# Optimization experiments

Measured on AMD Instinct MI355X. Metric: run time of the kernel, lower is better.

The kernel has to match this reference:

```python
import jax, jax.numpy as jnp
import numpy as np

BLOCK = 64      # base classifier input height/width
STRIDE = 16     # BLOCK // 4 per Windowing(stride=[1,bh/4,bw/4,1], size=[1,bh,bw,1])
K = 10          # n_classes
THRESH = 0.7    # bbox_threshold


def extract_patches(x):
    # x: [B,H,W,C] -> [B,R,Cc,BLOCK*BLOCK*C], same layout as tf.image.extract_patches
    B, H, Wd, C = x.shape
    R = (H - BLOCK) // STRIDE + 1
    Cc = (Wd - BLOCK) // STRIDE + 1
    rows = jnp.arange(R)[:, None] * STRIDE + jnp.arange(BLOCK)[None, :]   # [R,64]
    cols = jnp.arange(Cc)[:, None] * STRIDE + jnp.arange(BLOCK)[None, :]  # [Cc,64]
    p = x[:, rows]                 # [B,R,64,W,C]
    p = p[:, :, :, cols]           # [B,R,64,Cc,64,C]
    p = jnp.transpose(p, (0, 1, 3, 2, 4, 5))  # [B,R,Cc,64,64,C]
    return p.reshape(B, R, Cc, BLOCK * BLOCK * C)


def connected_components(mask):
    # 4-connected components of a 2D bool mask via iterative min-label propagation.
    # Background = 0; foreground labels are distinct positive ints per component.
    R, C = mask.shape
    big = jnp.int32(R * C + 2)
    init = jnp.where(mask, jnp.arange(1, R * C + 1, dtype=jnp.int32).reshape(R, C), 0)

    def step(lab, _):
        l = jnp.where(mask, lab, big)
        up = jnp.concatenate([jnp.full((1, C), big, l.dtype), l[:-1]], 0)
        dn = jnp.concatenate([l[1:], jnp.full((1, C), big, l.dtype)], 0)
        lf = jnp.concatenate([jnp.full((R, 1), big, l.dtype), l[:, :-1]], 1)
        rt = jnp.concatenate([l[:, 1:], jnp.full((R, 1), big, l.dtype)], 1)
        m = jnp.minimum(jnp.minimum(l, jnp.minimum(up, dn)), jnp.minimum(lf, rt))
        return jnp.where(mask, m, 0), None

    lab, _ = jax.lax.scan(step, init, None, length=2 * (R + C))
    return lab


def boxes_from_labels(lab):
    # Segmented min/max over label ids replaces the per-region python loop:
    # box = [rowmin-1, colmin-1, rowmax+1, colmax+1] per component.
    R, C = lab.shape
    N = R * C
    flat = lab.reshape(N)
    rr = jnp.arange(N, dtype=jnp.int32) // C
    cc = jnp.arange(N, dtype=jnp.int32) % C
    rmin = jax.ops.segment_min(rr, flat, num_segments=N + 1)
    cmin = jax.ops.segment_min(cc, flat, num_segments=N + 1)
    rmax = jax.ops.segment_max(rr, flat, num_segments=N + 1)
    cmax = jax.ops.segment_max(cc, flat, num_segments=N + 1)
    cnt = jax.ops.segment_sum(jnp.ones(N, jnp.int32), flat, num_segments=N + 1)
    valid = (cnt > 0).at[0].set(False)  # slot 0 is background
    boxes = jnp.stack([rmin - 1, cmin - 1, rmax + 1, cmax + 1], -1)
    boxes = jnp.where(valid[:, None], boxes, 0)
    return boxes, valid


def setup_inputs() -> dict:
    key = jax.random.key(0)
    k1, k2, k3 = jax.random.split(key, 3)
    inputs = jax.random.normal(k1, (1, 1024, 1024, 3), dtype=jnp.float32)
    # scale W so logits have ~unit variance -> sparse (realistic) threshold mask
    W = jax.random.normal(k2, (12288, K), dtype=jnp.float32) * 0.01
    b = jax.random.normal(k3, (K,), dtype=jnp.float32)
    return {"inputs": inputs, "W": W, "b": b}


def reference(inputs, W, b):
    patches = extract_patches(inputs)               # [1,R,Cc,D]
    B, R, Cc, D = patches.shape
    logits = patches.reshape(B * R * Cc, D) @ W + b # [N,K]
    prob = jax.nn.softmax(logits, axis=1).reshape(R, Cc, K)
    mask = prob > THRESH                            # [R,Cc,K]
    labels = jax.vmap(connected_components, in_axes=2, out_axes=2)(mask)  # [R,Cc,K]
    boxes, valid = jax.vmap(boxes_from_labels)(jnp.transpose(labels, (2, 0, 1)))
    # boxes: [K, R*Cc+1, 4] padded per-component bboxes; valid: [K, R*Cc+1]
    return prob, labels, boxes, valid
```

## Files before the change

kernel.cpp:

```cpp
#include <hip/hip_runtime.h>
#include <cmath>

#define KCLS 10
#define NCELL 3721
#define BIGV  0x0FFFFFFF

#define OUT_PROB 0
#define OUT_LAB  37210
#define OUT_BOX  74420
#define OUT_VALID 223300

#define XROW_PAD 3328

#define WF(q, n) ( ((n)&3)==0 ? (q)[(n)>>2].x : ((n)&3)==1 ? (q)[(n)>>2].y : \
                   ((n)&3)==2 ? (q)[(n)>>2].z : (q)[(n)>>2].w )

__global__ __launch_bounds__(256, 4) void k1a_partial(
    const float* __restrict__ x, const float* __restrict__ W,
    float* __restrict__ partial)
{
    const int tid  = threadIdx.x;
    const int bid  = blockIdx.x;
    const int i2   = bid / 61;
    const int r    = bid - i2 * 61;
    const int lane = tid & 63;
    const int tq   = tid >> 6;
    const int tqu  = __builtin_amdgcn_readfirstlane(tq);
    const int cc   = (lane < 61) ? lane : 60;

    __shared__ float xrow[2][XROW_PAD];
    __shared__ float red[4][61][KCLS];

#pragma unroll
    for (int ii = 0; ii < 2; ++ii) {
        const float* g = x + (size_t)((r << 4) + (i2 << 1) + ii) * 3072;
#pragma unroll
        for (int j = 0; j < 3; ++j) {
            const int idx = tid + (j << 8);
            const float4 v = *(const float4*)(g + (idx << 2));
            const int p = idx << 2;
            float* d = &xrow[ii][p + ((p / 48) << 2)];
            d[0] = v.x; d[1] = v.y; d[2] = v.z; d[3] = v.w;
        }
    }
    __syncthreads();

    float acc[KCLS];
#pragma unroll
    for (int k = 0; k < KCLS; ++k) acc[k] = 0.0f;

#pragma unroll
    for (int ii = 0; ii < 2; ++ii) {
        const int dbase = ((i2 << 1) + ii) * 192 + tqu * 48;
        const float* wrow = W + (size_t)dbase * KCLS;
        const float* lrow = &xrow[ii][52 * (cc + tqu)];
#pragma unroll
        for (int u = 0; u < 12; ++u) {
            const float4 xv = *(const float4*)(lrow + (u << 2));
            const float* wp = wrow + 40 * u;
            float4 wq[10];
#pragma unroll
            for (int j = 0; j < 10; ++j) wq[j] = *(const float4*)(wp + (j << 2));
#pragma unroll
            for (int k = 0; k < KCLS; ++k) {
                acc[k] += xv.x * WF(wq, k);
                acc[k] += xv.y * WF(wq, 10 + k);
                acc[k] += xv.z * WF(wq, 20 + k);
                acc[k] += xv.w * WF(wq, 30 + k);
            }
        }
    }

    if (lane < 61) {
#pragma unroll
        for (int k = 0; k < KCLS; ++k) red[tq][lane][k] = acc[k];
    }
    __syncthreads();

    for (int t = tid; t < 610; t += 256) {
        const int c = t / 10, k = t - c * 10;
        const float s = red[0][c][k] + red[1][c][k] + red[2][c][k] + red[3][c][k];
        partial[(size_t)i2 * 37210 + (size_t)r * 610 + (size_t)c * 10 + k] = s;
    }
}

__global__ __launch_bounds__(640) void k1b_softmax(
    const float* __restrict__ partial, const float* __restrict__ b,
    float* __restrict__ out)
{
    const int r   = blockIdx.x;
    const int tid = threadIdx.x;
    __shared__ double lgs[61][KCLS];

    if (tid < 610) {
        const int c = tid / 10, k = tid - c * 10;
        double s = (double)b[k];
        const float* p = partial + (size_t)r * 610 + tid;
#pragma unroll 8
        for (int i2 = 0; i2 < 32; ++i2)
            s += (double)p[(size_t)i2 * 37210];
        lgs[c][k] = s;
    }
    __syncthreads();

    if (tid < 61) {
        double l[KCLS];
#pragma unroll
        for (int k = 0; k < KCLS; ++k) l[k] = lgs[tid][k];
        double m = l[0];
#pragma unroll
        for (int k = 1; k < KCLS; ++k) m = fmax(m, l[k]);
        double e[KCLS], ssum = 0.0;
#pragma unroll
        for (int k = 0; k < KCLS; ++k) { e[k] = exp(l[k] - m); ssum += e[k]; }
        const double inv = 1.0 / ssum;
        float* po = out + OUT_PROB + (size_t)(r * 61 + tid) * KCLS;
#pragma unroll
        for (int k = 0; k < KCLS; ++k) po[k] = (float)(e[k] * inv);
    }
}

__global__ __launch_bounds__(1024) void k2_cc_boxes(float* __restrict__ out)
{
    const int k   = blockIdx.x;
    const int tid = threadIdx.x;

    __shared__ int lab[63 * 64];
    __shared__ int act[NCELL];
    __shared__ int nact, changed;
    __shared__ int rmn[NCELL + 1], rmx[NCELL + 1], cmn[NCELL + 1], cmx[NCELL + 1];

    for (int idx = tid; idx < 63 * 64; idx += 1024) lab[idx] = BIGV;
    for (int s = tid; s <= NCELL; s += 1024) {
        rmn[s] = 0x7fffffff; cmn[s] = 0x7fffffff; rmx[s] = -1; cmx[s] = -1;
    }
    if (tid == 0) nact = 0;
    __syncthreads();

    for (int idx = tid; idx < NCELL; idx += 1024) {
        const float pv = out[OUT_PROB + (size_t)idx * KCLS + k];
        if (pv > 0.7f) {
            const int r = idx / 61, c = idx - r * 61;
            const int off = (r + 1) * 64 + (c + 1);
            lab[off] = off;
            act[atomicAdd(&nact, 1)] = off;
        }
    }
    __syncthreads();
    const int na = nact;

    for (int round = 0; round < 128; ++round) {
        if (tid == 0) changed = 0;
        __syncthreads();
        bool ch = false;
        for (int ii = tid; ii < na; ii += 1024) {
            const int off = act[ii];
            const int v = lab[off];
            int m = v, t;
            t = lab[off - 1];  if (t < m) m = t;
            t = lab[off + 1];  if (t < m) m = t;
            t = lab[off - 64]; if (t < m) m = t;
            t = lab[off + 64]; if (t < m) m = t;
            if (m < v) {
                int p = lab[m];
                while (p < m) { m = p; p = lab[m]; }
                atomicMin(&lab[off], m);
                atomicMin(&lab[v],   m);
                ch = true;
            }
        }
        if (ch) changed = 1;
        __syncthreads();
        if (changed == 0) break;
        __syncthreads();
    }

    for (int idx = tid; idx < NCELL; idx += 1024) {
        const int r = idx / 61, c = idx - r * 61;
        const int v = lab[(r + 1) * 64 + (c + 1)];
        const int lv = (v < BIGV) ? ((v >> 6) * 61 - 61 + (v & 63)) : 0;
        out[OUT_LAB + (size_t)idx * KCLS + k] = (float)lv;
    }

    for (int ii = tid; ii < na; ii += 1024) {
        const int off = act[ii];
        const int v = lab[off];
        const int lb = (v >> 6) * 61 - 61 + (v & 63);
        const int r = (off >> 6) - 1, c = (off & 63) - 1;
        atomicMin(&rmn[lb], r); atomicMax(&rmx[lb], r);
        atomicMin(&cmn[lb], c); atomicMax(&cmx[lb], c);
    }
    __syncthreads();

    for (int s = tid; s <= NCELL; s += 1024) {
        const bool val = (s > 0) && (rmx[s] >= 0);
        float* bo = out + OUT_BOX + (size_t)(k * (NCELL + 1) + s) * 4;
        if (val) {
            bo[0] = (float)(rmn[s] - 1);
            bo[1] = (float)(cmn[s] - 1);
            bo[2] = (float)(rmx[s] + 1);
            bo[3] = (float)(cmx[s] + 1);
        } else {
            bo[0] = 0.0f; bo[1] = 0.0f; bo[2] = 0.0f; bo[3] = 0.0f;
        }
        out[OUT_VALID + (size_t)k * (NCELL + 1) + s] = val ? 1.0f : 0.0f;
    }
}

extern "C" void kernel_launch(void* const* d_in, const int* in_sizes, int n_in,
                              void* d_out, int out_size, void* d_ws, size_t ws_size,
                              hipStream_t stream) {
    const float* x = (const float*)d_in[0];
    const float* W = (const float*)d_in[1];
    const float* b = (const float*)d_in[2];
    float* out     = (float*)d_out;
    float* partial = (float*)d_ws;

    k1a_partial<<<dim3(1952), dim3(256), 0, stream>>>(x, W, partial);
    k1b_softmax<<<dim3(61),   dim3(640), 0, stream>>>(partial, b, out);
    k2_cc_boxes<<<dim3(KCLS), dim3(1024), 0, stream>>>(out);
}
```

Measured before the change: 93.76 us.

## Process two patch rows per block and stage W slice in LDS

Each k1a block now computes two patch rows instead of one, which halves the block count. The block's 384x10 W slice is loaded once into shared memory and reused for both rows, replacing per-thread global W reads. The four-wave reduction now uses LDS atomicAdd into a zero-initialized buffer instead of a staged sum. In exchange, per-thread register pressure roughly doubles (launch bounds drop to 2 blocks per SM), LDS use grows, and the float atomics make the summation order nondeterministic.

New measurement: 116.7 us. 24.5% more time.

```diff
diff --git a/kernel.cpp b/kernel.cpp
--- a/kernel.cpp
+++ b/kernel.cpp
@@ -15,72 +15,95 @@
 #define WF(q, n) ( ((n)&3)==0 ? (q)[(n)>>2].x : ((n)&3)==1 ? (q)[(n)>>2].y : \
                    ((n)&3)==2 ? (q)[(n)>>2].z : (q)[(n)>>2].w )
 
-__global__ __launch_bounds__(256, 4) void k1a_partial(
+__global__ __launch_bounds__(256, 2) void k1a_partial(
     const float* __restrict__ x, const float* __restrict__ W,
     float* __restrict__ partial)
 {
     const int tid  = threadIdx.x;
     const int bid  = blockIdx.x;
-    const int i2   = bid / 61;
-    const int r    = bid - i2 * 61;
+    const int i2   = bid / 31;
+    const int g    = bid - i2 * 31;
+    const int ra   = g * 2;
     const int lane = tid & 63;
     const int tq   = tid >> 6;
-    const int tqu  = __builtin_amdgcn_readfirstlane(tq);
     const int cc   = (lane < 61) ? lane : 60;
 
-    __shared__ float xrow[2][XROW_PAD];
-    __shared__ float red[4][61][KCLS];
+    __shared__ float xrow[2][2][XROW_PAD];
+    __shared__ float wlds[384 * KCLS];
+    __shared__ float red[2][61][KCLS];
+
+    for (int s = tid; s < 2 * 61 * KCLS; s += 256) ((float*)red)[s] = 0.0f;
+
+    {
+        const float* wsrc = W + (size_t)i2 * 3840;
+#pragma unroll
+        for (int j = 0; j < 4; ++j) {
+            const int idx = tid + (j << 8);
+            if (idx < 960)
+                *(float4*)(wlds + (idx << 2)) = *(const float4*)(wsrc + (idx << 2));
+        }
+    }
+#pragma unroll
+    for (int rr = 0; rr < 2; ++rr) {
+#pragma unroll
+        for (int ii = 0; ii < 2; ++ii) {
+            int prow = (ra + rr) * 16 + i2 * 2 + ii;
+            if (prow > 1023) prow = 1023;
+            const float* gp = x + (size_t)prow * 3072;
+#pragma unroll
+            for (int j = 0; j < 3; ++j) {
+                const int idx = tid + (j << 8);
+                const float4 v = *(const float4*)(gp + (idx << 2));
+                const int p = idx << 2;
+                float* d = &xrow[rr][ii][p + ((p / 48) << 2)];
+                d[0] = v.x; d[1] = v.y; d[2] = v.z; d[3] = v.w;
+            }
+        }
+    }
+    __syncthreads();
+
+    float accA[KCLS], accB[KCLS];
+#pragma unroll
+    for (int k = 0; k < KCLS; ++k) { accA[k] = 0.0f; accB[k] = 0.0f; }
 
 #pragma unroll
     for (int ii = 0; ii < 2; ++ii) {
-        const float* g = x + (size_t)((r << 4) + (i2 << 1) + ii) * 3072;
-#pragma unroll
-        for (int j = 0; j < 3; ++j) {
-            const int idx = tid + (j << 8);
-            const float4 v = *(const float4*)(g + (idx << 2));
-            const int p = idx << 2;
-            float* d = &xrow[ii][p + ((p / 48) << 2)];
-            d[0] = v.x; d[1] = v.y; d[2] = v.z; d[3] = v.w;
-        }
-    }
-    __syncthreads();
-
-    float acc[KCLS];
-#pragma unroll
-    for (int k = 0; k < KCLS; ++k) acc[k] = 0.0f;
-
-#pragma unroll
-    for (int ii = 0; ii < 2; ++ii) {
-        const int dbase = ((i2 << 1) + ii) * 192 + tqu * 48;
-        const float* wrow = W + (size_t)dbase * KCLS;
-        const float* lrow = &xrow[ii][52 * (cc + tqu)];
-#pragma unroll
+        const float* wl = wlds + (ii * 192 + tq * 48) * KCLS;
+        const float* lA = &xrow[0][ii][52 * (cc + tq)];
+        const float* lB = &xrow[1][ii][52 * (cc + tq)];
+#pragma unroll 2
         for (int u = 0; u < 12; ++u) {
-            const float4 xv = *(const float4*)(lrow + (u << 2));
-            const float* wp = wrow + 40 * u;
+            const float4 xa = *(const float4*)(lA + (u << 2));
+            const float4 xb = *(const float4*)(lB + (u << 2));
+            const float* wp = wl + 40 * u;
             float4 wq[10];
 #pragma unroll
-            for (int j = 0; j < 10; ++j) wq[j] = *(const float4*)(wp + (j << 2));
+            for (int q = 0; q < 10; ++q) wq[q] = *(const float4*)(wp + (q << 2));
 #pragma unroll
             for (int k = 0; k < KCLS; ++k) {
-                acc[k] += xv.x * WF(wq, k);
-                acc[k] += xv.y * WF(wq, 10 + k);
-                acc[k] += xv.z * WF(wq, 20 + k);
-                acc[k] += xv.w * WF(wq, 30 + k);
+                accA[k] += xa.x * WF(wq, k);       accB[k] += xb.x * WF(wq, k);
+                accA[k] += xa.y * WF(wq, 10 + k);  accB[k] += xb.y * WF(wq, 10 + k);
+                accA[k] += xa.z * WF(wq, 20 + k);  accB[k] += xb.z * WF(wq, 20 + k);
+                accA[k] += xa.w * WF(wq, 30 + k);  accB[k] += xb.w * WF(wq, 30 + k);
             }
         }
     }
 
     if (lane < 61) {
 #pragma unroll
-        for (int k = 0; k < KCLS; ++k) red[tq][lane][k] = acc[k];
-    }
-    __syncthreads();
-
-    for (int t = tid; t < 610; t += 256) {
-        const int c = t / 10, k = t - c * 10;
-        const float s = red[0][c][k] + red[1][c][k] + red[2][c][k] + red[3][c][k];
-        partial[(size_t)i2 * 37210 + (size_t)r * 610 + (size_t)c * 10 + k] = s;
+        for (int k = 0; k < KCLS; ++k) {
+            atomicAdd(&red[0][cc][k], accA[k]);
+            atomicAdd(&red[1][cc][k], accB[k]);
+        }
+    }
+    __syncthreads();
+
+    for (int t = tid; t < 610; t += 256)
+        partial[(size_t)i2 * 37210 + (size_t)ra * 610 + t] = ((const float*)red)[t];
+    if (ra + 1 <= 60) {
+        for (int t = tid; t < 610; t += 256)
+            partial[(size_t)i2 * 37210 + (size_t)(ra + 1) * 610 + t]
+                = ((const float*)red)[610 + t];
     }
 }
 
@@ -216,7 +239,7 @@
     float* out     = (float*)d_out;
     float* partial = (float*)d_ws;
 
-    k1a_partial<<<dim3(1952), dim3(256), 0, stream>>>(x, W, partial);
-    k1b_softmax<<<dim3(61),   dim3(640), 0, stream>>>(partial, b, out);
+    k1a_partial<<<dim3(992), dim3(256), 0, stream>>>(x, W, partial);
+    k1b_softmax<<<dim3(61),  dim3(640), 0, stream>>>(partial, b, out);
     k2_cc_boxes<<<dim3(KCLS), dim3(1024), 0, stream>>>(out);
 }
```
